# Optimization experiments

Measured on AMD Instinct MI355X. Metric: run time of the kernel, lower is better.

Reference implementation:

```python
import jax, jax.numpy as jnp
import numpy as np

NX = 48
NY = 48
K0DX = 0.2026833935483871
N_PML = 8
_PI = 3.1415926


def _fun_s(u):
    # PML stretch factor s(u) = kappa(u) + 1j*sigma_over_omega(u)
    power_kappa = 3
    kappa_max = 15
    power_sigma = 3
    lambda_over_dx = 40
    sigma_over_omega_max = 0.8 * (power_sigma + 1) * lambda_over_dx / (2 * _PI)
    return (1.0 + (kappa_max - 1) * u ** power_kappa) + 1j * (sigma_over_omega_max * u ** power_sigma)


def _lap1d_pml(N, N_L, N_R):
    # 1D second-difference operator with stretched-coordinate PML (dense numpy, constant)
    ddx1 = np.eye(N + 1, N) - np.eye(N + 1, N, k=-1)   # forward difference (N+1, N)
    ddx2 = -ddx1.T                                      # (N, N+1)
    s_half = np.ones(N + 1, dtype=np.complex128)
    s_int = np.ones(N, dtype=np.complex128)
    if N_R > 0:
        s_half[N - N_R:N + 1] = _fun_s(np.arange(0.5, N_R + 1, 1.0) / (N_R + 1))
        s_int[N - N_R:N] = _fun_s(np.arange(1.0, N_R + 1, 1.0) / (N_R + 1))
    if N_L > 0:
        s_half[N_L::-1] = _fun_s(np.arange(0.5, N_L + 1, 1.0) / (N_L + 1))
        s_int[N_L - 1::-1] = _fun_s(np.arange(1.0, N_L + 1, 1.0) / (N_L + 1))
    return np.diag(1.0 / s_int) @ ddx2 @ np.diag(1.0 / s_half) @ ddx1


def _build_A1():
    # 2D Helmholtz Laplacian with PML: kron(Ax, I) + kron(I, Ay), dense 2304x2304 complex64
    Ax = _lap1d_pml(NX, N_PML, N_PML)
    Ay = _lap1d_pml(NY, N_PML, N_PML)
    return (np.kron(Ax, np.eye(NY)) + np.kron(np.eye(NX), Ay)).astype(np.complex64)


_A1 = _build_A1()  # constant system matrix part


def setup_inputs() -> dict:
    key = jax.random.key(0)
    k1, k2, k3, k4, k5 = jax.random.split(key, 5)
    return {
        "n_prediction": jax.random.uniform(k1, (1, NX, NY, 1), dtype=jnp.float32),
        "n_predict_allresults": jax.random.normal(k2, (1, NX, NY, 1), dtype=jnp.float32),
        "x_b": jax.random.normal(k3, (1, NX, NY, 1), dtype=jnp.float32),
        "y_aim": jax.random.normal(k4, (1, NX, NY, 2), dtype=jnp.float32),
        "simulation_region": jax.random.normal(k5, (1, NX, NY, 1), dtype=jnp.float32),
    }


def reference(n_prediction, n_predict_allresults, x_b, y_aim, simulation_region):
    A1 = jnp.asarray(_A1)  # (2304, 2304) complex64
    # A = A1 + k0dx^2 * diag(n^2), with n flattened after [0,2,1,3] transpose
    n_c = n_prediction.astype(jnp.complex64)
    n_flat = jnp.transpose(n_c, (0, 2, 1, 3)).reshape(-1)  # (2304,)
    A = A1 + jnp.diag((K0DX ** 2) * n_flat ** 2)
    # RHS b, same transpose+flatten convention
    b = jnp.transpose(x_b.astype(jnp.complex64), (0, 2, 1, 3)).reshape(NX * NY, 1)
    # Dense complex linear solve A psi = b
    psi = jnp.linalg.solve(A, b).reshape(1, NX, NY, 1)
    psi_tot = jnp.transpose(psi, (0, 2, 1, 3))  # (1, 48, 48, 1) complex64
    y_c = y_aim.astype(jnp.complex64)
    err1 = psi_tot * y_c[:, :, :, 0:1]
    err2 = psi_tot * y_c[:, :, :, 1:2]
    en1 = y_c[:, :, :, 0:1] * y_c[:, :, :, 0:1]
    en2 = y_c[:, :, :, 1:2] * y_c[:, :, :, 1:2]
    return jnp.concatenate([err1, err2, en1, en2], axis=-1)  # (1, 48, 48, 4) complex64
```

## Files before the change

kernel.cpp:

```cpp
#include <hip/hip_runtime.h>


#define NXY 48
#define NN  2304

typedef float v2 __attribute__((ext_vector_type(2)));
typedef double2 zplx;

__device__ __forceinline__ v2 mk2(float x, float y){ v2 r; r.x=x; r.y=y; return r; }
__device__ __forceinline__ v2 bcx(v2 a){ return __builtin_shufflevector(a,a,0,0); }
__device__ __forceinline__ v2 bcy(v2 a){ return __builtin_shufflevector(a,a,1,1); }
__device__ __forceinline__ v2 jswp(v2 a){ v2 r = __builtin_shufflevector(a,a,1,0); r.x = -r.x; return r; }
__device__ __forceinline__ v2 cmul(v2 a, v2 b){
    return __builtin_elementwise_fma(bcx(a), b, bcy(a)*jswp(b));
}
__device__ __forceinline__ v2 cfma_(v2 c, v2 a, v2 b){
    return __builtin_elementwise_fma(bcx(a), b, __builtin_elementwise_fma(bcy(a), jswp(b), c));
}
__device__ __forceinline__ v2 cfms(v2 c, v2 a, v2 b){
    return __builtin_elementwise_fma(-bcx(a), b, __builtin_elementwise_fma(-bcy(a), jswp(b), c));
}
__device__ __forceinline__ v2 cinv(v2 a){
    float s = 1.0f/fmaf(a.x,a.x, a.y*a.y);
    return mk2(a.x*s, -a.y*s);
}
__device__ __forceinline__ v2 shfl_c(v2 a, int lane){
    return mk2(__shfl(a.x, lane), __shfl(a.y, lane));
}
__device__ __forceinline__ v2 bfly_c(v2 v){
    v.x += __shfl_xor(v.x,1); v.y += __shfl_xor(v.y,1);
    v.x += __shfl_xor(v.x,2); v.y += __shfl_xor(v.y,2);
    v.x += __shfl_xor(v.x,4); v.y += __shfl_xor(v.y,4);
    return v;
}

__device__ __forceinline__ zplx zmul64(zplx a, zplx b){
    return make_double2(a.x*b.x - a.y*b.y, a.x*b.y + a.y*b.x);
}
__device__ __forceinline__ zplx zadd64(zplx a, zplx b){ return make_double2(a.x+b.x, a.y+b.y); }
__device__ __forceinline__ zplx zneg64(zplx a){ return make_double2(-a.x, -a.y); }
__device__ __forceinline__ zplx zinv64(zplx a){
    double s = 1.0/(a.x*a.x + a.y*a.y);
    return make_double2(a.x*s, -a.y*s);
}
__device__ __forceinline__ zplx fun_s(double u){
    const double sig = 0.8*4.0*40.0/(2.0*3.1415926);
    double u3 = u*u*u;
    return make_double2(1.0 + 14.0*u3, sig*u3);
}
__device__ __forceinline__ zplx s_half_at(int j){
    if (j <= 8)  return fun_s((8.5 - (double)j)/9.0);
    if (j >= 40) return fun_s(((double)(j-40) + 0.5)/9.0);
    return make_double2(1.0, 0.0);
}
__device__ __forceinline__ zplx s_int_at(int j){
    if (j <= 7)  return fun_s((8.0 - (double)j)/9.0);
    if (j >= 40) return fun_s(((double)(j-40) + 1.0)/9.0);
    return make_double2(1.0, 0.0);
}

__device__ __forceinline__ void gj48(v2 (&m)[6][6], const int lr, const int lc){
    v2 pv, rs[6], cs[6];
    {
        const int rsrc0 = lc, csrc0 = (lr<<3);
        pv = shfl_c(m[0][0], 0);
        #pragma unroll
        for (int j=0;j<6;++j) rs[j] = shfl_c(m[0][j], rsrc0);
        #pragma unroll
        for (int i=0;i<6;++i) cs[i] = shfl_c(m[i][0], csrc0);
    }
    #pragma unroll 1
    for (int kr=0; kr<8; ++kr){
        const bool prow = (lr==kr), pcol = (lc==kr);
        #pragma unroll
        for (int kj=0; kj<6; ++kj){
            const int nj = (kj+1)%6;
            const int cr = (kj==5) ? ((kr<7)?(kr+1):7) : kr;
            const int nrsrc = (cr<<3)|lc;
            const int ncsrc = (lr<<3)|cr;
            const int ndsrc = (cr<<3)|cr;
            v2 d = cinv(pv);
            v2 rsp[6];
            #pragma unroll
            for (int j=0;j<6;++j) rsp[j] = cmul(d, rs[j]);
            if (pcol) rsp[kj] = d + mk2(1.f,0.f);
            v2 u[6];
            #pragma unroll
            for (int i=0;i<6;++i) u[i] = cs[i];
            if (prow) u[kj] = pv - mk2(1.f,0.f);
            #pragma unroll
            for (int j=0;j<6;++j) m[nj][j] = cfms(m[nj][j], u[nj], rsp[j]);
            #pragma unroll
            for (int i=0;i<6;++i){ if (i!=nj) m[i][nj] = cfms(m[i][nj], u[i], rsp[nj]); }
            v2 npv = shfl_c(m[nj][nj], ndsrc);
            v2 nrs[6], ncs[6];
            #pragma unroll
            for (int j=0;j<6;++j) nrs[j] = shfl_c(m[nj][j], nrsrc);
            #pragma unroll
            for (int i=0;i<6;++i) ncs[i] = shfl_c(m[i][nj], ncsrc);
            #pragma unroll
            for (int i=0;i<6;++i){
                if (i==nj) continue;
                #pragma unroll
                for (int j=0;j<6;++j){
                    if (j==nj) continue;
                    m[i][j] = cfms(m[i][j], u[i], rsp[j]);
                }
            }
            pv = npv;
            #pragma unroll
            for (int j=0;j<6;++j){ rs[j]=nrs[j]; cs[j]=ncs[j]; }
        }
    }
}

__global__ __launch_bounds__(128,1) void helm_babe(
    const float* __restrict__ n_pred,
    const float* __restrict__ xb,
    const float* __restrict__ yaim,
    float*       __restrict__ out,
    int                       out_size,
    float*       __restrict__ wsG)
{
    __shared__ v2 dgv[NXY], lov[NXY], hiv[NXY];
    __shared__ float nk[NN];
    __shared__ float bb[NN];
    __shared__ v2 zv[NN];
    __shared__ v2 Hx[NN];
    __shared__ v2 vv[NXY];

    const int t    = threadIdx.x;
    const int lane = t & 63;
    const int wid  = t >> 6;
    const int lr = lane>>3, lc = lane&7;
    const int r0 = 6*lr, c0v = 6*lc;
    const int diagl = (lc<<3)|lc;
    const double k2 = 0.2026833935483871*0.2026833935483871;

    if (t < NXY){
        int a = t;
        zplx isha  = zinv64(s_half_at(a));
        zplx isha1 = zinv64(s_half_at(a+1));
        zplx isi   = zinv64(s_int_at(a));
        zplx dgd = zneg64(zmul64(isi, zadd64(isha,isha1)));
        zplx lod = zmul64(isi, isha);
        zplx hid = zmul64(isi, isha1);
        dgv[a] = mk2((float)dgd.x,(float)dgd.y);
        lov[a] = mk2((float)lod.x,(float)lod.y);
        hiv[a] = mk2((float)hid.x,(float)hid.y);
    }
    for (int e=t; e<NN; e+=128){
        int i_=e/48, a_=e%48;
        float nv = n_pred[a_*48+i_];
        nk[e] = (float)(k2*(double)nv*(double)nv);
        bb[e] = xb[a_*48+i_];
    }
    __syncthreads();

    const int dir    = (wid==0) ? 1 : -1;
    const int ibeg   = (wid==0) ? 0 : 47;
    const int nsteps = (wid==0) ? 25 : 23;

    v2 g[6][6];
    v2 m[6][6];
    v2 zrow[6];
    #pragma unroll
    for (int i=0;i<6;++i) zrow[i] = mk2(0.f,0.f);

    #pragma unroll 1
    for (int step=0; step<nsteps; ++step){
        int ib = ibeg + dir*step;
        bool full = !(wid==0 && step==24);

        v2 zc[6];
        #pragma unroll
        for (int j=0;j<6;++j) zc[j] = shfl_c(zrow[j], diagl);

        v2 nci = mk2(0.f,0.f), czp = mk2(0.f,0.f);
        if (step>0){
            if (dir>0){ nci = cmul(lov[ib], hiv[ib-1]); czp = lov[ib]; }
            else      { nci = cmul(hiv[ib], lov[ib+1]); czp = hiv[ib]; }
            nci = -nci;
        }
        bool same  = (lc==lr), rightn = (lc==lr+1), leftn = (lc+1==lr);
        v2 p[6];
        #pragma unroll
        for (int i=0;i<6;++i){
            int r = r0+i;
            v2 dgr = dgv[r], lor = lov[r], hir = hiv[r];
            v2 ddi = dgv[ib] + dgr + mk2(nk[ib*48+r],0.f);
            v2 acc = mk2(0.f,0.f);
            #pragma unroll
            for (int j=0;j<6;++j){
                v2 v = (step>0)? cmul(nci, g[i][j]) : mk2(0.f,0.f);
                if (same){
                    if (j==i)   v = v + ddi;
                    if (j==i+1) v = v + hir;
                    if (j+1==i) v = v + lor;
                }
                if (rightn && i==5 && j==0) v = v + hir;
                if (leftn  && i==0 && j==5) v = v + lor;
                m[i][j] = v;
                if (step>0) acc = cfma_(acc, g[i][j], zc[j]);
            }
            p[i] = acc;
        }
        if (step>0){
            #pragma unroll
            for (int i=0;i<6;++i){
                v2 w = bfly_c(p[i]);
                zrow[i] = cfms(mk2(bb[ib*48+r0+i],0.f), czp, w);
            }
        } else {
            #pragma unroll
            for (int i=0;i<6;++i) zrow[i] = mk2(bb[ib*48+r0+i], 0.f);
        }
        if (lc==0){
            #pragma unroll
            for (int i=0;i<6;++i) zv[ib*48+r0+i] = zrow[i];
        }

        if (full){
            gj48(m, lr, lc);
            if (ib == 25){
                #pragma unroll
                for (int i=0;i<6;++i)
                    #pragma unroll
                    for (int j=0;j<6;++j) Hx[(r0+i)*48 + c0v + j] = m[i][j];
            } else {
                #pragma unroll
                for (int i=0;i<6;++i){
                    float4* w4 = (float4*)(wsG + 2*((size_t)ib*NN + (r0+i)*48 + c0v));
                    #pragma unroll
                    for (int jp=0;jp<3;++jp){
                        float4 f;
                        f.x = m[i][2*jp].x;   f.y = m[i][2*jp].y;
                        f.z = m[i][2*jp+1].x; f.w = m[i][2*jp+1].y;
                        w4[jp] = f;
                    }
                }
            }
            #pragma unroll
            for (int i=0;i<6;++i)
                #pragma unroll
                for (int j=0;j<6;++j) g[i][j] = m[i][j];
        }
    }

    if (wid==1){
        v2 zc[6];
        #pragma unroll
        for (int j=0;j<6;++j) zc[j] = shfl_c(zrow[j], diagl);
        #pragma unroll
        for (int i=0;i<6;++i){
            v2 acc = mk2(0.f,0.f);
            #pragma unroll
            for (int j=0;j<6;++j) acc = cfma_(acc, m[i][j], zc[j]);
            acc = bfly_c(acc);
            if (lc==0) vv[r0+i] = acc;
        }
    }
    __syncthreads();

    v2 xrow[6];
    if (wid==0){
        v2 cf = cmul(hiv[24], lov[25]);
        #pragma unroll
        for (int i=0;i<6;++i)
            #pragma unroll
            for (int j=0;j<6;++j) m[i][j] = cfms(m[i][j], cf, Hx[(r0+i)*48 + c0v + j]);
        #pragma unroll
        for (int i=0;i<6;++i) zrow[i] = cfms(zrow[i], hiv[24], vv[r0+i]);
        gj48(m, lr, lc);
        v2 zc[6];
        #pragma unroll
        for (int j=0;j<6;++j) zc[j] = shfl_c(zrow[j], diagl);
        #pragma unroll
        for (int i=0;i<6;++i){
            v2 acc = mk2(0.f,0.f);
            #pragma unroll
            for (int j=0;j<6;++j) acc = cfma_(acc, m[i][j], zc[j]);
            xrow[i] = bfly_c(acc);
        }
        if (lc==0){
            #pragma unroll
            for (int i=0;i<6;++i) zv[24*48+r0+i] = xrow[i];
        }
        v2 xc[6], tm[6];
        #pragma unroll
        for (int j=0;j<6;++j) xc[j] = shfl_c(xrow[j], diagl);
        #pragma unroll
        for (int j=0;j<6;++j) tm[j] = cfms(zv[25*48+c0v+j], lov[25], xc[j]);
        #pragma unroll
        for (int i=0;i<6;++i){
            v2 acc = mk2(0.f,0.f);
            #pragma unroll
            for (int j=0;j<6;++j) acc = cfma_(acc, Hx[(r0+i)*48 + c0v + j], tm[j]);
            acc = bfly_c(acc);
            if (lc==0) zv[25*48+r0+i] = acc;
        }
    }
    __syncthreads();

    if (wid==0){
        #pragma unroll 1
        for (int ib=23; ib>=0; --ib){
            v2 xc[6], tm[6];
            #pragma unroll
            for (int j=0;j<6;++j) xc[j] = shfl_c(xrow[j], diagl);
            v2 hiib = hiv[ib];
            #pragma unroll
            for (int j=0;j<6;++j) tm[j] = cfms(zv[ib*48+c0v+j], hiib, xc[j]);
            #pragma unroll
            for (int i=0;i<6;++i){
                const float4* w4 = (const float4*)(wsG + 2*((size_t)ib*NN + (r0+i)*48 + c0v));
                v2 acc = mk2(0.f,0.f);
                #pragma unroll
                for (int jp=0;jp<3;++jp){
                    float4 f = w4[jp];
                    acc = cfma_(acc, mk2(f.x,f.y), tm[2*jp]);
                    acc = cfma_(acc, mk2(f.z,f.w), tm[2*jp+1]);
                }
                xrow[i] = bfly_c(acc);
            }
            if (lc==0){
                #pragma unroll
                for (int i=0;i<6;++i) zv[ib*48+r0+i] = xrow[i];
            }
        }
    } else {
        #pragma unroll
        for (int i=0;i<6;++i) xrow[i] = zv[25*48+r0+i];
        #pragma unroll 1
        for (int ib=26; ib<NXY; ++ib){
            v2 xc[6], tm[6];
            #pragma unroll
            for (int j=0;j<6;++j) xc[j] = shfl_c(xrow[j], diagl);
            v2 loib = lov[ib];
            #pragma unroll
            for (int j=0;j<6;++j) tm[j] = cfms(zv[ib*48+c0v+j], loib, xc[j]);
            #pragma unroll
            for (int i=0;i<6;++i){
                const float4* w4 = (const float4*)(wsG + 2*((size_t)ib*NN + (r0+i)*48 + c0v));
                v2 acc = mk2(0.f,0.f);
                #pragma unroll
                for (int jp=0;jp<3;++jp){
                    float4 f = w4[jp];
                    acc = cfma_(acc, mk2(f.x,f.y), tm[2*jp]);
                    acc = cfma_(acc, mk2(f.z,f.w), tm[2*jp+1]);
                }
                xrow[i] = bfly_c(acc);
            }
            if (lc==0){
                #pragma unroll
                for (int i=0;i<6;++i) zv[ib*48+r0+i] = xrow[i];
            }
        }
    }
    __syncthreads();

    for (int e=t; e<NN; e+=128){
        int alpha=e/48, beta=e%48;
        v2 psi = zv[beta*48+alpha];
        float y0=yaim[2*e], y1=yaim[2*e+1];
        if (out_size == NN*4){
            float4 o = make_float4(psi.x*y0, psi.x*y1, y0*y0, y1*y1);
            *(float4*)(out + 4*e) = o;
        } else {
            float* o = out + 8*e;
            o[0]=psi.x*y0; o[1]=psi.y*y0; o[2]=psi.x*y1; o[3]=psi.y*y1;
            o[4]=y0*y0; o[5]=0.f; o[6]=y1*y1; o[7]=0.f;
        }
    }
}

extern "C" void kernel_launch(void* const* d_in, const int* in_sizes, int n_in,
                              void* d_out, int out_size, void* d_ws, size_t ws_size,
                              hipStream_t stream) {
    const float* n_pred = (const float*)d_in[0];
    const float* xb     = (const float*)d_in[2];
    const float* ya     = (const float*)d_in[3];
    float* out = (float*)d_out;
    float* wsG = (float*)d_ws;

    hipLaunchKernelGGL(helm_babe, dim3(1), dim3(128), 0, stream,
                       n_pred, xb, ya, out, out_size, wsG);
}
```

Before: 614.8 us.

## Broadcast Gauss-Jordan pivot row/column via LDS instead of cross-lane shuffles

The in-register 48x48 Gauss-Jordan inversion used to broadcast the pivot row, pivot column and pivot element to all lanes with many per-element shuffles every pivot step. It now has the owning lanes write the next pivot row and column as packed float4 values into double-buffered per-wave LDS buffers, and all lanes read them back. The identity adjustments and the scaling by the pivot inverse are folded into those stores and into precomputed U values. This replaces about 13 shuffles per step with a few LDS stores and vector loads, but relies on wave-synchronous LDS visibility without explicit barriers and adds LDS latency on the critical path.

Result: slower. 632.7 us (+2.9%).

```diff
diff --git a/kernel.cpp b/kernel.cpp
--- a/kernel.cpp
+++ b/kernel.cpp
@@ -5,6 +5,7 @@
 #define NN  2304
 
 typedef float v2 __attribute__((ext_vector_type(2)));
+typedef float v4 __attribute__((ext_vector_type(4)));
 typedef double2 zplx;
 
 __device__ __forceinline__ v2 mk2(float x, float y){ v2 r; r.x=x; r.y=y; return r; }
@@ -59,57 +60,99 @@
     return make_double2(1.0, 0.0);
 }
 
-__device__ __forceinline__ void gj48(v2 (&m)[6][6], const int lr, const int lc){
-    v2 pv, rs[6], cs[6];
+__device__ __forceinline__ void gj48_lds(v2 (&m)[6][6], const int lr, const int lc,
+                                         v4* Rb, v4* Cb, v2* Dp){
+    v2 R[6], U[6];
+    if (lr==0){
+        #pragma unroll
+        for (int jp=0;jp<3;++jp){
+            v2 a = m[0][2*jp], b = m[0][2*jp+1];
+            if (lc==0 && jp==0) a.x += 1.f;
+            v4 t; t.x=a.x; t.y=a.y; t.z=b.x; t.w=b.y;
+            Rb[3*lc+jp] = t;
+        }
+    }
+    if (lc==0){
+        #pragma unroll
+        for (int ip=0;ip<3;++ip){
+            v2 a = m[2*ip][0], b = m[2*ip+1][0];
+            if (lr==0 && ip==0) a.x -= 1.f;
+            v4 t; t.x=a.x; t.y=a.y; t.z=b.x; t.w=b.y;
+            Cb[3*lr+ip] = t;
+        }
+        if (lr==0) Dp[0] = m[0][0];
+    }
+    __builtin_amdgcn_sched_barrier(0);
     {
-        const int rsrc0 = lc, csrc0 = (lr<<3);
-        pv = shfl_c(m[0][0], 0);
-        #pragma unroll
-        for (int j=0;j<6;++j) rs[j] = shfl_c(m[0][j], rsrc0);
-        #pragma unroll
-        for (int i=0;i<6;++i) cs[i] = shfl_c(m[i][0], csrc0);
+        v2 pvd = Dp[0];
+        v4 rt0 = Rb[3*lc+0], rt1 = Rb[3*lc+1], rt2 = Rb[3*lc+2];
+        v4 ct0 = Cb[3*lr+0], ct1 = Cb[3*lr+1], ct2 = Cb[3*lr+2];
+        v2 d = cinv(pvd);
+        R[0]=mk2(rt0.x,rt0.y); R[1]=mk2(rt0.z,rt0.w);
+        R[2]=mk2(rt1.x,rt1.y); R[3]=mk2(rt1.z,rt1.w);
+        R[4]=mk2(rt2.x,rt2.y); R[5]=mk2(rt2.z,rt2.w);
+        U[0]=cmul(d,mk2(ct0.x,ct0.y)); U[1]=cmul(d,mk2(ct0.z,ct0.w));
+        U[2]=cmul(d,mk2(ct1.x,ct1.y)); U[3]=cmul(d,mk2(ct1.z,ct1.w));
+        U[4]=cmul(d,mk2(ct2.x,ct2.y)); U[5]=cmul(d,mk2(ct2.z,ct2.w));
     }
     #pragma unroll 1
     for (int kr=0; kr<8; ++kr){
-        const bool prow = (lr==kr), pcol = (lc==kr);
         #pragma unroll
         for (int kj=0; kj<6; ++kj){
-            const int nj = (kj+1)%6;
-            const int cr = (kj==5) ? ((kr<7)?(kr+1):7) : kr;
-            const int nrsrc = (cr<<3)|lc;
-            const int ncsrc = (lr<<3)|cr;
-            const int ndsrc = (cr<<3)|cr;
-            v2 d = cinv(pv);
-            v2 rsp[6];
-            #pragma unroll
-            for (int j=0;j<6;++j) rsp[j] = cmul(d, rs[j]);
-            if (pcol) rsp[kj] = d + mk2(1.f,0.f);
-            v2 u[6];
-            #pragma unroll
-            for (int i=0;i<6;++i) u[i] = cs[i];
-            if (prow) u[kj] = pv - mk2(1.f,0.f);
-            #pragma unroll
-            for (int j=0;j<6;++j) m[nj][j] = cfms(m[nj][j], u[nj], rsp[j]);
-            #pragma unroll
-            for (int i=0;i<6;++i){ if (i!=nj) m[i][nj] = cfms(m[i][nj], u[i], rsp[nj]); }
-            v2 npv = shfl_c(m[nj][nj], ndsrc);
-            v2 nrs[6], ncs[6];
-            #pragma unroll
-            for (int j=0;j<6;++j) nrs[j] = shfl_c(m[nj][j], nrsrc);
-            #pragma unroll
-            for (int i=0;i<6;++i) ncs[i] = shfl_c(m[i][nj], ncsrc);
+            const int nj   = (kj==5) ? 0 : (kj+1);
+            const int ncr  = (kj==5) ? ((kr<7)?(kr+1):7) : kr;
+            const int boff = 24*(nj&1);
+            const int dsel = nj&1;
+            #pragma unroll
+            for (int j=0;j<6;++j) m[nj][j] = cfms(m[nj][j], U[nj], R[j]);
+            #pragma unroll
+            for (int i=0;i<6;++i){ if (i!=nj) m[i][nj] = cfms(m[i][nj], U[i], R[nj]); }
+            if (lr==ncr){
+                #pragma unroll
+                for (int jp=0;jp<3;++jp){
+                    v2 a = m[nj][2*jp], b = m[nj][2*jp+1];
+                    if (lc==ncr){
+                        if (2*jp==nj)   a.x += 1.f;
+                        if (2*jp+1==nj) b.x += 1.f;
+                    }
+                    v4 t; t.x=a.x; t.y=a.y; t.z=b.x; t.w=b.y;
+                    Rb[boff+3*lc+jp] = t;
+                }
+            }
+            if (lc==ncr){
+                #pragma unroll
+                for (int ip=0;ip<3;++ip){
+                    v2 a = m[2*ip][nj], b = m[2*ip+1][nj];
+                    if (lr==ncr){
+                        if (2*ip==nj)   a.x -= 1.f;
+                        if (2*ip+1==nj) b.x -= 1.f;
+                    }
+                    v4 t; t.x=a.x; t.y=a.y; t.z=b.x; t.w=b.y;
+                    Cb[boff+3*lr+ip] = t;
+                }
+                if (lr==ncr) Dp[dsel] = m[nj][nj];
+            }
+            __builtin_amdgcn_sched_barrier(0);
+            v2 pvd = Dp[dsel];
+            v4 rt0 = Rb[boff+3*lc+0], rt1 = Rb[boff+3*lc+1], rt2 = Rb[boff+3*lc+2];
+            v4 ct0 = Cb[boff+3*lr+0], ct1 = Cb[boff+3*lr+1], ct2 = Cb[boff+3*lr+2];
+            __builtin_amdgcn_sched_barrier(0);
             #pragma unroll
             for (int i=0;i<6;++i){
                 if (i==nj) continue;
                 #pragma unroll
                 for (int j=0;j<6;++j){
                     if (j==nj) continue;
-                    m[i][j] = cfms(m[i][j], u[i], rsp[j]);
-                }
-            }
-            pv = npv;
-            #pragma unroll
-            for (int j=0;j<6;++j){ rs[j]=nrs[j]; cs[j]=ncs[j]; }
+                    m[i][j] = cfms(m[i][j], U[i], R[j]);
+                }
+            }
+            v2 d = cinv(pvd);
+            R[0]=mk2(rt0.x,rt0.y); R[1]=mk2(rt0.z,rt0.w);
+            R[2]=mk2(rt1.x,rt1.y); R[3]=mk2(rt1.z,rt1.w);
+            R[4]=mk2(rt2.x,rt2.y); R[5]=mk2(rt2.z,rt2.w);
+            U[0]=cmul(d,mk2(ct0.x,ct0.y)); U[1]=cmul(d,mk2(ct0.z,ct0.w));
+            U[2]=cmul(d,mk2(ct1.x,ct1.y)); U[3]=cmul(d,mk2(ct1.z,ct1.w));
+            U[4]=cmul(d,mk2(ct2.x,ct2.y)); U[5]=cmul(d,mk2(ct2.z,ct2.w));
         }
     }
 }
@@ -128,6 +171,9 @@
     __shared__ v2 zv[NN];
     __shared__ v2 Hx[NN];
     __shared__ v2 vv[NXY];
+    __shared__ v4 Rbuf[2][48];
+    __shared__ v4 Cbuf[2][48];
+    __shared__ v2 Dbuf[2][2];
 
     const int t    = threadIdx.x;
     const int lane = t & 63;
@@ -136,6 +182,10 @@
     const int r0 = 6*lr, c0v = 6*lc;
     const int diagl = (lc<<3)|lc;
     const double k2 = 0.2026833935483871*0.2026833935483871;
+
+    v4* Rb = &Rbuf[wid][0];
+    v4* Cb = &Cbuf[wid][0];
+    v2* Dp = &Dbuf[wid][0];
 
     if (t < NXY){
         int a = t;
@@ -221,7 +271,7 @@
         }
 
         if (full){
-            gj48(m, lr, lc);
+            gj48_lds(m, lr, lc, Rb, Cb, Dp);
             if (ib == 25){
                 #pragma unroll
                 for (int i=0;i<6;++i)
@@ -271,7 +321,7 @@
             for (int j=0;j<6;++j) m[i][j] = cfms(m[i][j], cf, Hx[(r0+i)*48 + c0v + j]);
         #pragma unroll
         for (int i=0;i<6;++i) zrow[i] = cfms(zrow[i], hiv[24], vv[r0+i]);
-        gj48(m, lr, lc);
+        gj48_lds(m, lr, lc, Rb, Cb, Dp);
         v2 zc[6];
         #pragma unroll
         for (int j=0;j<6;++j) zc[j] = shfl_c(zrow[j], diagl);
```

## Block Gauss-Jordan by 2x2 pivots with LDS row/column broadcast

Applied to the files above, without the earlier changes.

Replaces the rank-1 in-register Gauss-Jordan inversion of each 48x48 block with a rank-2 (2x2 pivot block) variant. Pivot rows, columns and the 2x2 pivot block are broadcast through double-buffered per-wavefront shared memory instead of per-element cross-lane shuffles. This halves the number of pivot steps and the serialized shuffle/inverse chain per step. In exchange it adds LDS traffic, relies on wave-synchronous visibility without explicit barriers, and uses 2x2 block pivots without pivoting, which may change numerical stability.

Result: slower. 676.9 us (+10.1%).

```diff
diff --git a/kernel.cpp b/kernel.cpp
--- a/kernel.cpp
+++ b/kernel.cpp
@@ -5,6 +5,7 @@
 #define NN  2304
 
 typedef float v2 __attribute__((ext_vector_type(2)));
+typedef float v4 __attribute__((ext_vector_type(4)));
 typedef double2 zplx;
 
 __device__ __forceinline__ v2 mk2(float x, float y){ v2 r; r.x=x; r.y=y; return r; }
@@ -59,57 +60,139 @@
     return make_double2(1.0, 0.0);
 }
 
-__device__ __forceinline__ void gj48(v2 (&m)[6][6], const int lr, const int lc){
-    v2 pv, rs[6], cs[6];
+__device__ __forceinline__ void gj48_lds(v2 (&m)[6][6], const int lr, const int lc,
+                                         v4* Rb, v4* Cb, v4* Pb){
+    v2 R2[2][6], U2[6][2];
+    if (lr==0){
+        #pragma unroll
+        for (int j=0;j<6;++j){
+            v2 a = m[0][j], b = m[1][j];
+            if (lc==0){
+                if (j==0) a.x += 1.f;
+                if (j==1) b.x += 1.f;
+            }
+            v4 t; t.x=a.x; t.y=a.y; t.z=b.x; t.w=b.y;
+            Rb[6*lc+j] = t;
+        }
+    }
+    if (lc==0){
+        #pragma unroll
+        for (int i=0;i<6;++i){
+            v2 a = m[i][0], b = m[i][1];
+            if (lr==0){
+                if (i==0) a.x -= 1.f;
+                if (i==1) b.x -= 1.f;
+            }
+            v4 t; t.x=a.x; t.y=a.y; t.z=b.x; t.w=b.y;
+            Cb[6*lr+i] = t;
+        }
+        if (lr==0){
+            v4 t0; t0.x=m[0][0].x; t0.y=m[0][0].y; t0.z=m[0][1].x; t0.w=m[0][1].y;
+            v4 t1; t1.x=m[1][0].x; t1.y=m[1][0].y; t1.z=m[1][1].x; t1.w=m[1][1].y;
+            Pb[0] = t0; Pb[1] = t1;
+        }
+    }
+    __builtin_amdgcn_sched_barrier(0);
     {
-        const int rsrc0 = lc, csrc0 = (lr<<3);
-        pv = shfl_c(m[0][0], 0);
-        #pragma unroll
-        for (int j=0;j<6;++j) rs[j] = shfl_c(m[0][j], rsrc0);
-        #pragma unroll
-        for (int i=0;i<6;++i) cs[i] = shfl_c(m[i][0], csrc0);
+        v4 p0 = Pb[0], p1 = Pb[1];
+        v4 rt[6], ct[6];
+        #pragma unroll
+        for (int j=0;j<6;++j) rt[j] = Rb[6*lc+j];
+        #pragma unroll
+        for (int i=0;i<6;++i) ct[i] = Cb[6*lr+i];
+        v2 P00=mk2(p0.x,p0.y), P01=mk2(p0.z,p0.w), P10=mk2(p1.x,p1.y), P11=mk2(p1.z,p1.w);
+        v2 det = cfms(cmul(P00,P11), P01, P10);
+        v2 id  = cinv(det);
+        v2 D00 = cmul(P11,id), D11 = cmul(P00,id);
+        v2 D01 = -cmul(P01,id), D10 = -cmul(P10,id);
+        #pragma unroll
+        for (int j=0;j<6;++j){ R2[0][j]=mk2(rt[j].x,rt[j].y); R2[1][j]=mk2(rt[j].z,rt[j].w); }
+        #pragma unroll
+        for (int i=0;i<6;++i){
+            v2 c0 = mk2(ct[i].x,ct[i].y), c1 = mk2(ct[i].z,ct[i].w);
+            U2[i][0] = cfma_(cmul(c0,D00), c1, D10);
+            U2[i][1] = cfma_(cmul(c0,D01), c1, D11);
+        }
     }
     #pragma unroll 1
     for (int kr=0; kr<8; ++kr){
-        const bool prow = (lr==kr), pcol = (lc==kr);
-        #pragma unroll
-        for (int kj=0; kj<6; ++kj){
-            const int nj = (kj+1)%6;
-            const int cr = (kj==5) ? ((kr<7)?(kr+1):7) : kr;
-            const int nrsrc = (cr<<3)|lc;
-            const int ncsrc = (lr<<3)|cr;
-            const int ndsrc = (cr<<3)|cr;
-            v2 d = cinv(pv);
-            v2 rsp[6];
-            #pragma unroll
-            for (int j=0;j<6;++j) rsp[j] = cmul(d, rs[j]);
-            if (pcol) rsp[kj] = d + mk2(1.f,0.f);
-            v2 u[6];
-            #pragma unroll
-            for (int i=0;i<6;++i) u[i] = cs[i];
-            if (prow) u[kj] = pv - mk2(1.f,0.f);
-            #pragma unroll
-            for (int j=0;j<6;++j) m[nj][j] = cfms(m[nj][j], u[nj], rsp[j]);
-            #pragma unroll
-            for (int i=0;i<6;++i){ if (i!=nj) m[i][nj] = cfms(m[i][nj], u[i], rsp[nj]); }
-            v2 npv = shfl_c(m[nj][nj], ndsrc);
-            v2 nrs[6], ncs[6];
-            #pragma unroll
-            for (int j=0;j<6;++j) nrs[j] = shfl_c(m[nj][j], nrsrc);
-            #pragma unroll
-            for (int i=0;i<6;++i) ncs[i] = shfl_c(m[i][nj], ncsrc);
-            #pragma unroll
-            for (int i=0;i<6;++i){
-                if (i==nj) continue;
+        #pragma unroll
+        for (int kp=0; kp<3; ++kp){
+            const int np  = (kp==2) ? 0 : (kp+1);
+            const int e0  = 2*np, e1 = e0+1;
+            const int ncr = (kp==2) ? ((kr<7)?(kr+1):7) : kr;
+            const int ps  = (kr + kp + 1) & 1;
+            const int bo  = 48*ps;
+            #pragma unroll
+            for (int j=0;j<6;++j){
+                m[e0][j] = cfms(cfms(m[e0][j], U2[e0][0], R2[0][j]), U2[e0][1], R2[1][j]);
+                m[e1][j] = cfms(cfms(m[e1][j], U2[e1][0], R2[0][j]), U2[e1][1], R2[1][j]);
+            }
+            #pragma unroll
+            for (int i=0;i<6;++i){
+                if (i==e0 || i==e1) continue;
+                m[i][e0] = cfms(cfms(m[i][e0], U2[i][0], R2[0][e0]), U2[i][1], R2[1][e0]);
+                m[i][e1] = cfms(cfms(m[i][e1], U2[i][0], R2[0][e1]), U2[i][1], R2[1][e1]);
+            }
+            if (lr==ncr){
                 #pragma unroll
                 for (int j=0;j<6;++j){
-                    if (j==nj) continue;
-                    m[i][j] = cfms(m[i][j], u[i], rsp[j]);
-                }
-            }
-            pv = npv;
-            #pragma unroll
-            for (int j=0;j<6;++j){ rs[j]=nrs[j]; cs[j]=ncs[j]; }
+                    v2 a = m[e0][j], b = m[e1][j];
+                    if (lc==ncr){
+                        if (j==e0) a.x += 1.f;
+                        if (j==e1) b.x += 1.f;
+                    }
+                    v4 t; t.x=a.x; t.y=a.y; t.z=b.x; t.w=b.y;
+                    Rb[bo+6*lc+j] = t;
+                }
+            }
+            if (lc==ncr){
+                #pragma unroll
+                for (int i=0;i<6;++i){
+                    v2 a = m[i][e0], b = m[i][e1];
+                    if (lr==ncr){
+                        if (i==e0) a.x -= 1.f;
+                        if (i==e1) b.x -= 1.f;
+                    }
+                    v4 t; t.x=a.x; t.y=a.y; t.z=b.x; t.w=b.y;
+                    Cb[bo+6*lr+i] = t;
+                }
+                if (lr==ncr){
+                    v4 t0; t0.x=m[e0][e0].x; t0.y=m[e0][e0].y; t0.z=m[e0][e1].x; t0.w=m[e0][e1].y;
+                    v4 t1; t1.x=m[e1][e0].x; t1.y=m[e1][e0].y; t1.z=m[e1][e1].x; t1.w=m[e1][e1].y;
+                    Pb[2*ps+0] = t0; Pb[2*ps+1] = t1;
+                }
+            }
+            __builtin_amdgcn_sched_barrier(0);
+            v4 p0 = Pb[2*ps+0], p1 = Pb[2*ps+1];
+            v4 rt[6], ct[6];
+            #pragma unroll
+            for (int j=0;j<6;++j) rt[j] = Rb[bo+6*lc+j];
+            #pragma unroll
+            for (int i=0;i<6;++i) ct[i] = Cb[bo+6*lr+i];
+            __builtin_amdgcn_sched_barrier(0);
+            #pragma unroll
+            for (int i=0;i<6;++i){
+                if (i==e0 || i==e1) continue;
+                #pragma unroll
+                for (int j=0;j<6;++j){
+                    if (j==e0 || j==e1) continue;
+                    m[i][j] = cfms(cfms(m[i][j], U2[i][0], R2[0][j]), U2[i][1], R2[1][j]);
+                }
+            }
+            v2 P00=mk2(p0.x,p0.y), P01=mk2(p0.z,p0.w), P10=mk2(p1.x,p1.y), P11=mk2(p1.z,p1.w);
+            v2 det = cfms(cmul(P00,P11), P01, P10);
+            v2 id  = cinv(det);
+            v2 D00 = cmul(P11,id), D11 = cmul(P00,id);
+            v2 D01 = -cmul(P01,id), D10 = -cmul(P10,id);
+            #pragma unroll
+            for (int j=0;j<6;++j){ R2[0][j]=mk2(rt[j].x,rt[j].y); R2[1][j]=mk2(rt[j].z,rt[j].w); }
+            #pragma unroll
+            for (int i=0;i<6;++i){
+                v2 c0 = mk2(ct[i].x,ct[i].y), c1 = mk2(ct[i].z,ct[i].w);
+                U2[i][0] = cfma_(cmul(c0,D00), c1, D10);
+                U2[i][1] = cfma_(cmul(c0,D01), c1, D11);
+            }
         }
     }
 }
@@ -128,6 +211,9 @@
     __shared__ v2 zv[NN];
     __shared__ v2 Hx[NN];
     __shared__ v2 vv[NXY];
+    __shared__ v4 Rbuf[2][96];
+    __shared__ v4 Cbuf[2][96];
+    __shared__ v4 Pbuf[2][4];
 
     const int t    = threadIdx.x;
     const int lane = t & 63;
@@ -136,6 +222,10 @@
     const int r0 = 6*lr, c0v = 6*lc;
     const int diagl = (lc<<3)|lc;
     const double k2 = 0.2026833935483871*0.2026833935483871;
+
+    v4* Rb = &Rbuf[wid][0];
+    v4* Cb = &Cbuf[wid][0];
+    v4* Pb = &Pbuf[wid][0];
 
     if (t < NXY){
         int a = t;
@@ -221,7 +311,7 @@
         }
 
         if (full){
-            gj48(m, lr, lc);
+            gj48_lds(m, lr, lc, Rb, Cb, Pb);
             if (ib == 25){
                 #pragma unroll
                 for (int i=0;i<6;++i)
@@ -271,7 +361,7 @@
             for (int j=0;j<6;++j) m[i][j] = cfms(m[i][j], cf, Hx[(r0+i)*48 + c0v + j]);
         #pragma unroll
         for (int i=0;i<6;++i) zrow[i] = cfms(zrow[i], hiv[24], vv[r0+i]);
-        gj48(m, lr, lc);
+        gj48_lds(m, lr, lc, Rb, Cb, Pb);
         v2 zc[6];
         #pragma unroll
         for (int j=0;j<6;++j) zc[j] = shfl_c(zrow[j], diagl);
```
